# Performance work log

Hardware: AMD Instinct MI355X
Metric: run time of the kernel (lower is better)

Reference implementation:

```python
import jax, jax.numpy as jnp
import numpy as np

N, IN_DIM, OUT_DIM, BATCH = 8192, 128, 128, 4


def _glorot(key, shape):
    lim = float(np.sqrt(6.0 / (shape[0] + shape[1])))
    return jax.random.uniform(key, shape, jnp.float32, -lim, lim)


def setup_inputs() -> dict:
    key = jax.random.key(0)
    ks = jax.random.split(key, 16)
    inp = {
        "x": jax.random.normal(ks[0], (BATCH, N, IN_DIM), jnp.float32),
        "L0": jax.random.normal(ks[1], (N, N), jnp.float32) / np.sqrt(N),
        "L1": jax.random.normal(ks[2], (N, N), jnp.float32) / np.sqrt(N),
        "L2": jax.random.normal(ks[3], (N, N), jnp.float32) / np.sqrt(N),
        "L3": jax.random.normal(ks[4], (N, N), jnp.float32) / np.sqrt(N),
    }
    # 8 GCN layers: (branch b, layer l) -> W_bl, bias_bl
    kidx = 5
    for b in range(4):
        for l in range(2):
            d_in = IN_DIM if l == 0 else OUT_DIM
            inp[f"W{b}{l}"] = _glorot(ks[kidx], (d_in, OUT_DIM))
            inp[f"b{b}{l}"] = jnp.zeros((OUT_DIM,), jnp.float32)
            kidx += 1
    return inp


def _gcn_block(L, x, W, b):
    # support = L @ x  (graph propagation), then dense transform + ReLU
    support = jnp.einsum("nm,bmf->bnf", L, x)  # [B, N, F_in]
    return jax.nn.relu(support @ W + b)        # [B, N, F_out]


def reference(x, L0, L1, L2, L3,
              W00, b00, W01, b01,
              W10, b10, W11, b11,
              W20, b20, W21, b21,
              W30, b30, W31, b31):
    x0 = _gcn_block(L0, _gcn_block(L0, x, W00, b00), W01, b01)
    x1 = _gcn_block(L1, _gcn_block(L1, x, W10, b10), W11, b11)
    x2 = _gcn_block(L2, _gcn_block(L2, x, W20, b20), W21, b21)
    x3 = _gcn_block(L3, _gcn_block(L3, x, W30, b30), W31, b31)
    return (x0, x1, x2, x3)
```

## Files before the change

kernel.cpp:

```cpp
#include <hip/hip_runtime.h>
#include <stdint.h>


typedef short bf16x8 __attribute__((ext_vector_type(8)));
typedef float f32x4 __attribute__((ext_vector_type(4)));

static __device__ __forceinline__ unsigned short f2bf(float f) {
  __bf16 h = (__bf16)f;
  return __builtin_bit_cast(unsigned short, h);
}
static __device__ __forceinline__ unsigned int pack2(float a, float b) {
  return (unsigned int)f2bf(a) | ((unsigned int)f2bf(b) << 16);
}
static __device__ __forceinline__ bf16x8 cvt8(float4 lo, float4 hi) {
  bf16x8 r;
  r[0] = (short)f2bf(lo.x); r[1] = (short)f2bf(lo.y);
  r[2] = (short)f2bf(lo.z); r[3] = (short)f2bf(lo.w);
  r[4] = (short)f2bf(hi.x); r[5] = (short)f2bf(hi.y);
  r[6] = (short)f2bf(hi.z); r[7] = (short)f2bf(hi.w);
  return r;
}

#define GLOAD16(g, l)                                                                  \
  __builtin_amdgcn_global_load_lds((const __attribute__((address_space(1))) void*)(g), \
                                   (__attribute__((address_space(3))) void*)(l), 16, 0, 0)

struct WPtrs { const float* w[8]; };
__global__ __launch_bounds__(256)
void prep_w(WPtrs p, unsigned short* __restrict__ wt) {
  const int s = blockIdx.x;
  const float* W = p.w[s];
  unsigned short* dst = wt + s * 16384;
  for (int i = threadIdx.x; i < 16384; i += 256) {
    const int fi = i >> 7, fo = i & 127;
    dst[fo * 128 + fi] = f2bf(W[i]);
  }
}

template <int AFP32>
__global__ __launch_bounds__(256)
void small_gemm(const float* __restrict__ x, const unsigned short* __restrict__ H1m,
                const unsigned short* __restrict__ WT, unsigned short* __restrict__ Z) {
  __shared__ unsigned short Sa[128 * 136];

  const int t = threadIdx.x, lane = t & 63, wave = t >> 6;
  const int l15 = lane & 15, lk = (lane >> 4) * 8;
  const int wm = (wave >> 1) * 64, wn = (wave & 1) * 64;
  const int mt = blockIdx.x, br = blockIdx.y;
  const int batch = mt >> 6, node0 = (mt & 63) * 128;

  {
    const int row = t >> 1, seg = (t & 1) * 64;
    if (AFP32) {
      const float4* src = (const float4*)(x + ((size_t)batch * 8192 + node0 + row) * 128 + seg);
      uint4* dst = (uint4*)&Sa[row * 136 + seg];
#pragma unroll
      for (int i = 0; i < 8; ++i) {
        float4 a = src[i * 2], b = src[i * 2 + 1];
        uint4 v;
        v.x = pack2(a.x, a.y); v.y = pack2(a.z, a.w);
        v.z = pack2(b.x, b.y); v.w = pack2(b.z, b.w);
        dst[i] = v;
      }
    } else {
      const uint4* src = (const uint4*)(H1m + ((size_t)(br * 4 + batch) * 8192 + node0 + row) * 128 + seg);
      uint4* dst = (uint4*)&Sa[row * 136 + seg];
#pragma unroll
      for (int i = 0; i < 8; ++i) dst[i] = src[i];
    }
  }
  __syncthreads();

  const unsigned short* WTb = WT + (size_t)(2 * br + (AFP32 ? 0 : 1)) * 16384;
  f32x4 acc[4][4];
#pragma unroll
  for (int i = 0; i < 4; ++i)
#pragma unroll
    for (int j = 0; j < 4; ++j) acc[i][j] = f32x4{0.f, 0.f, 0.f, 0.f};

#pragma unroll
  for (int kk = 0; kk < 4; ++kk) {
    bf16x8 av[4], wv[4];
#pragma unroll
    for (int mi = 0; mi < 4; ++mi)
      av[mi] = *(const bf16x8*)&Sa[(wm + mi * 16 + l15) * 136 + kk * 32 + lk];
#pragma unroll
    for (int ni = 0; ni < 4; ++ni)
      wv[ni] = *(const bf16x8*)&WTb[(wn + ni * 16 + l15) * 128 + kk * 32 + lk];
#pragma unroll
    for (int mi = 0; mi < 4; ++mi)
#pragma unroll
      for (int ni = 0; ni < 4; ++ni)
        acc[mi][ni] = __builtin_amdgcn_mfma_f32_16x16x32_bf16(av[mi], wv[ni], acc[mi][ni], 0, 0, 0);
  }

#pragma unroll
  for (int mi = 0; mi < 4; ++mi) {
#pragma unroll
    for (int ni = 0; ni < 4; ++ni) {
      const int row0 = wm + mi * 16 + (lane >> 4) * 4;
      const int col  = wn + ni * 16 + l15;
      uint2 pv;
      pv.x = pack2(acc[mi][ni][0], acc[mi][ni][1]);
      pv.y = pack2(acc[mi][ni][2], acc[mi][ni][3]);
      *(uint2*)(Z + ((size_t)br * 512 + batch * 128 + col) * 8192 + node0 + row0) = pv;
    }
  }
}

struct BigArgs {
  const float* L[4];
  const float* bias[4];
  const unsigned short* Z;
  void* Dst;
};

template <int LAYER>
__global__ __launch_bounds__(512, 2)
void big_gemm(BigArgs a) {
  extern __shared__ char smem[];

  const int t = threadIdx.x, lane = t & 63, wave = t >> 6;
  const int l15 = lane & 15;
  const int wm = (wave >> 2) * 128, wn = (wave & 3) * 64;

  const int bid = blockIdx.x;
  const int work = (bid & 7) * 32 + (bid >> 3);
  const int nb = work & 1, mt = (work >> 1) & 31, br = work >> 6;
  const int mbase = mt * 256;

  const float* A = a.L[br];
  const float* bias = a.bias[br];
  const unsigned short* Zb = a.Z + (size_t)br * (512 * 8192);

  const int c0 = 2 * (lane & 1);
  const int akey = (lane >> 2) & 3;
  const float* aBase = A + (size_t)(mbase + wave * 32 + (lane >> 1)) * 8192 + c0 * 8;
  char* aLane = smem + (wave * 32 + (lane >> 1)) * 64;
  const unsigned short* bG = Zb + (size_t)(nb * 256 + wave * 32 + (lane >> 2)) * 8192
                                + ((lane & 3) ^ ((lane >> 3) & 3)) * 8;
  char* bWave = smem + 65536 + wave * 2048;

  const int aoff = (((lane >> 4) ^ ((lane >> 1) & 3)) & 7) * 16;

  f32x4 acc[8][4];
#pragma unroll
  for (int i = 0; i < 8; ++i)
#pragma unroll
    for (int j = 0; j < 4; ++j) acc[i][j] = f32x4{0.f, 0.f, 0.f, 0.f};

  float4 ra[4], rb[4];

#define GLB(s)                                              \
  do {                                                      \
    const unsigned short* bp = bG + (size_t)(s) * 32;       \
    char* bl = bWave + ((s) & 3) * 16384;                   \
    GLOAD16(bp, bl);                                        \
    GLOAD16(bp + 16 * 8192, bl + 1024);                     \
  } while (0)

#define LOADA(s, R)                                         \
  do {                                                      \
    const float* ap = aBase + (size_t)(s) * 32;             \
    R[0] = *(const float4*)(ap);                            \
    R[1] = *(const float4*)(ap + 4);                        \
    R[2] = *(const float4*)(ap + 8);                        \
    R[3] = *(const float4*)(ap + 12);                       \
  } while (0)

#define WRITEA(s, R)                                                        \
  do {                                                                      \
    char* al = aLane + ((s) & 3) * 16384;                                   \
    *(bf16x8*)(al + ((c0 ^ akey) * 16)) = cvt8(R[0], R[1]);                 \
    *(bf16x8*)(al + (((c0 + 1) ^ akey) * 16)) = cvt8(R[2], R[3]);           \
  } while (0)

#define MFMA_HALF(NLO)                                                                         \
  do {                                                                                         \
    __builtin_amdgcn_s_setprio(1);                                                             \
    _Pragma("unroll") for (int mi = 0; mi < 8; ++mi) {                                         \
      acc[mi][NLO] = __builtin_amdgcn_mfma_f32_16x16x32_bf16(av[mi], bv[0], acc[mi][NLO], 0, 0, 0); \
      acc[mi][NLO + 1] = __builtin_amdgcn_mfma_f32_16x16x32_bf16(av[mi], bv[1], acc[mi][NLO + 1], 0, 0, 0); \
    }                                                                                          \
    __builtin_amdgcn_s_setprio(0);                                                             \
  } while (0)

#define ITER(T_, PREV_, NEXT_, VMSTR_, DO_GLB_, DO_LOADA_, DO_WRITEA_)                  \
  do {                                                                                  \
    asm volatile("s_waitcnt lgkmcnt(0)" ::: "memory");                                  \
    __builtin_amdgcn_s_barrier();                                                       \
    asm volatile("" ::: "memory");                                                      \
    if (DO_GLB_) GLB((T_) + 3);                                                         \
    if (DO_LOADA_) LOADA((T_) + 2, NEXT_);                                              \
    const char* ab = smem + ((T_) & 3) * 16384;                                         \
    const char* bb = smem + 65536 + ((T_) & 3) * 16384;                                 \
    bf16x8 av[8], bv[2];                                                                \
    _Pragma("unroll") for (int mi = 0; mi < 8; ++mi)                                    \
        av[mi] = *(const bf16x8*)(ab + (wm + mi * 16 + l15) * 64 + aoff);               \
    bv[0] = *(const bf16x8*)(bb + (wn + l15) * 64 + aoff);                              \
    bv[1] = *(const bf16x8*)(bb + (wn + 16 + l15) * 64 + aoff);                         \
    MFMA_HALF(0);                                                                       \
    if (DO_WRITEA_) {                                                                   \
      asm volatile("s_waitcnt " VMSTR_ ::: "memory");                                   \
      WRITEA((T_) + 1, PREV_);                                                          \
    }                                                                                   \
    bv[0] = *(const bf16x8*)(bb + (wn + 32 + l15) * 64 + aoff);                         \
    bv[1] = *(const bf16x8*)(bb + (wn + 48 + l15) * 64 + aoff);                         \
    MFMA_HALF(2);                                                                       \
  } while (0)

  GLB(0); GLB(1); GLB(2);
  LOADA(0, ra); LOADA(1, rb);
  WRITEA(0, ra);

  for (int tt = 0; tt < 252; tt += 2) {
    ITER(tt,     rb, ra, "vmcnt(6)", 1, 1, 1);
    ITER(tt + 1, ra, rb, "vmcnt(6)", 1, 1, 1);
  }
  ITER(252, rb, ra, "vmcnt(6)", 1, 1, 1);
  ITER(253, ra, rb, "vmcnt(4)", 0, 1, 1);
  ITER(254, rb, ra, "vmcnt(0)", 0, 0, 1);
  {
    asm volatile("s_waitcnt lgkmcnt(0)" ::: "memory");
    __builtin_amdgcn_s_barrier();
    asm volatile("" ::: "memory");
    const char* ab = smem + (255 & 3) * 16384;
    const char* bb = smem + 65536 + (255 & 3) * 16384;
    bf16x8 av[8], bv[2];
#pragma unroll
    for (int mi = 0; mi < 8; ++mi)
      av[mi] = *(const bf16x8*)(ab + (wm + mi * 16 + l15) * 64 + aoff);
    bv[0] = *(const bf16x8*)(bb + (wn + l15) * 64 + aoff);
    bv[1] = *(const bf16x8*)(bb + (wn + 16 + l15) * 64 + aoff);
    MFMA_HALF(0);
    bv[0] = *(const bf16x8*)(bb + (wn + 32 + l15) * 64 + aoff);
    bv[1] = *(const bf16x8*)(bb + (wn + 48 + l15) * 64 + aoff);
    MFMA_HALF(2);
  }
#undef ITER
#undef MFMA_HALF
#undef WRITEA
#undef LOADA
#undef GLB

  asm volatile("s_waitcnt lgkmcnt(0)" ::: "memory");
  __builtin_amdgcn_s_barrier();
  asm volatile("" ::: "memory");

  unsigned short* S16 = (unsigned short*)smem;
  float* S32 = (float*)smem;

#pragma unroll
  for (int h = 0; h < 2; ++h) {
    if (((wave >> 1) & 1) == h) {
#pragma unroll
      for (int mi = 0; mi < 8; ++mi) {
#pragma unroll
        for (int ni = 0; ni < 4; ++ni) {
          const int row0 = wm + mi * 16 + (lane >> 4) * 4;
          const int col  = (wave & 1) * 64 + ni * 16 + l15;
          const float bvv = bias[col];
#pragma unroll
          for (int r = 0; r < 4; ++r) {
            const float v = fmaxf(acc[mi][ni][r] + bvv, 0.f);
            if (LAYER == 0) S16[(row0 + r) * 136 + col] = f2bf(v);
            else            S32[(row0 + r) * 128 + col] = v;
          }
        }
      }
    }
    __syncthreads();
    const int batch = nb * 2 + h;
    const int row = t >> 1, seg = (t & 1) * 64;
    if (LAYER == 0) {
      unsigned short* Dst = (unsigned short*)a.Dst;
      const uint4* src = (const uint4*)&S16[row * 136 + seg];
      uint4* dst = (uint4*)(Dst + ((size_t)(br * 4 + batch) * 8192 + mbase + row) * 128 + seg);
#pragma unroll
      for (int i = 0; i < 8; ++i) dst[i] = src[i];
    } else {
      float* Dst = (float*)a.Dst;
      const float4* src = (const float4*)&S32[row * 128 + seg];
      float4* dst = (float4*)(Dst + ((size_t)(br * 4 + batch) * 8192 + mbase + row) * 128 + seg);
#pragma unroll
      for (int i = 0; i < 16; ++i) dst[i] = src[i];
    }
    __syncthreads();
  }
}

extern "C" void kernel_launch(void* const* d_in, const int* in_sizes, int n_in,
                              void* d_out, int out_size, void* d_ws, size_t ws_size,
                              hipStream_t stream) {
  const float* x = (const float*)d_in[0];
  unsigned short* Z   = (unsigned short*)d_ws;
  unsigned short* H1m = Z + (size_t)4 * 512 * 8192;
  unsigned short* WT  = H1m + (size_t)4 * 4 * 8192 * 128;
  float* out = (float*)d_out;

  static int attr_done = 0;
  if (!attr_done) {
    hipFuncSetAttribute((const void*)big_gemm<0>, hipFuncAttributeMaxDynamicSharedMemorySize, 131072);
    hipFuncSetAttribute((const void*)big_gemm<1>, hipFuncAttributeMaxDynamicSharedMemorySize, 131072);
    attr_done = 1;
  }

  WPtrs wp;
  for (int b = 0; b < 4; ++b) {
    wp.w[b * 2 + 0] = (const float*)d_in[5 + b * 4 + 0];
    wp.w[b * 2 + 1] = (const float*)d_in[5 + b * 4 + 2];
  }
  prep_w<<<8, 256, 0, stream>>>(wp, WT);

  BigArgs a0, a1;
  for (int b = 0; b < 4; ++b) {
    a0.L[b] = (const float*)d_in[1 + b];
    a1.L[b] = (const float*)d_in[1 + b];
    a0.bias[b] = (const float*)d_in[6 + b * 4];
    a1.bias[b] = (const float*)d_in[8 + b * 4];
  }
  a0.Z = Z; a0.Dst = (void*)H1m;
  a1.Z = Z; a1.Dst = (void*)out;

  small_gemm<1><<<dim3(256, 4), 256, 0, stream>>>(x, nullptr, WT, Z);
  big_gemm<0><<<256, 512, 131072, stream>>>(a0);
  small_gemm<0><<<dim3(256, 4), 256, 0, stream>>>(nullptr, H1m, WT, Z);
  big_gemm<1><<<256, 512, 131072, stream>>>(a1);
}
```

Measured before the change: 1.032 ms.

## Rewrite big GEMM main loop with 32x32x16 MFMA and 64-wide K stages

Replaces the 16x16x32 MFMA tiling with 32x32x16 bf16 MFMAs, so each wave holds eight 32x32 accumulators. The K loop now stages 64-wide A and B slices, with A double-buffered in registers and B triple-buffered in LDS, using 160KB of shared memory and new XOR swizzles. The point is to cut LDS fragment reads per FLOP and issue denser MFMA work. In exchange it adds two barriers per phase, drops the min-2-blocks launch bound, and needs more LDS per block.

Result: slower. 1.776 ms (+72.1%).

```diff
diff --git a/kernel.cpp b/kernel.cpp
--- a/kernel.cpp
+++ b/kernel.cpp
@@ -3,7 +3,8 @@
 
 
 typedef short bf16x8 __attribute__((ext_vector_type(8)));
-typedef float f32x4 __attribute__((ext_vector_type(4)));
+typedef float f32x4  __attribute__((ext_vector_type(4)));
+typedef float f32x16 __attribute__((ext_vector_type(16)));
 
 static __device__ __forceinline__ unsigned short f2bf(float f) {
   __bf16 h = (__bf16)f;
@@ -116,12 +117,12 @@
 };
 
 template <int LAYER>
-__global__ __launch_bounds__(512, 2)
+__global__ __launch_bounds__(512)
 void big_gemm(BigArgs a) {
   extern __shared__ char smem[];
 
   const int t = threadIdx.x, lane = t & 63, wave = t >> 6;
-  const int l15 = lane & 15;
+  const int l31 = lane & 31, hk = lane >> 5;
   const int wm = (wave >> 2) * 128, wn = (wave & 3) * 64;
 
   const int bid = blockIdx.x;
@@ -133,141 +134,137 @@
   const float* bias = a.bias[br];
   const unsigned short* Zb = a.Z + (size_t)br * (512 * 8192);
 
-  const int c0 = 2 * (lane & 1);
-  const int akey = (lane >> 2) & 3;
-  const float* aBase = A + (size_t)(mbase + wave * 32 + (lane >> 1)) * 8192 + c0 * 8;
-  char* aLane = smem + (wave * 32 + (lane >> 1)) * 64;
-  const unsigned short* bG = Zb + (size_t)(nb * 256 + wave * 32 + (lane >> 2)) * 8192
-                                + ((lane & 3) ^ ((lane >> 3) & 3)) * 8;
-  char* bWave = smem + 65536 + wave * 2048;
-
-  const int aoff = (((lane >> 4) ^ ((lane >> 1) & 3)) & 7) * 16;
-
-  f32x4 acc[8][4];
-#pragma unroll
-  for (int i = 0; i < 8; ++i)
-#pragma unroll
-    for (int j = 0; j < 4; ++j) acc[i][j] = f32x4{0.f, 0.f, 0.f, 0.f};
-
-  float4 ra[4], rb[4];
-
-#define GLB(s)                                              \
-  do {                                                      \
-    const unsigned short* bp = bG + (size_t)(s) * 32;       \
-    char* bl = bWave + ((s) & 3) * 16384;                   \
-    GLOAD16(bp, bl);                                        \
-    GLOAD16(bp + 16 * 8192, bl + 1024);                     \
+  const int arow = t >> 1, ah = t & 1;
+  const float* aG = A + (size_t)(mbase + arow) * 8192 + ah * 32;
+  const int awBase = arow * 128, awKey = arow & 7, ah4 = ah * 4;
+  const int brow = lane >> 3;
+  const unsigned short* bG = Zb + (size_t)(nb * 256 + wave * 32 + brow) * 8192
+                                + ((lane & 7) ^ (brow & 7)) * 8;
+  const int bW = wave * 4096;
+
+  const int aBase = (wm + l31) * 128;
+  const int bBase = (wn + l31) * 128;
+  const int key7 = l31 & 7;
+
+  f32x16 c00{}, c01{}, c10{}, c11{}, c20{}, c21{}, c30{}, c31{};
+  float4 E[8], O[8];
+  bf16x8 av0, av1, av2, av3, bv0, bv1;
+
+#define A_LD(SET, KOFF, q) do {                              \
+    const float* _p = aG + (KOFF) + (q) * 8;                 \
+    SET[2 * (q)]     = *(const float4*)_p;                   \
+    SET[2 * (q) + 1] = *(const float4*)(_p + 4); } while (0)
+
+#define A_WR(SET, SLOT, q) do {                              \
+    *(bf16x8*)(smem + (SLOT) * 32768 + awBase +              \
+               (((ah4 + (q)) ^ awKey) * 16)) =               \
+        cvt8(SET[2 * (q)], SET[2 * (q) + 1]); } while (0)
+
+#define B_ST(KOFF, BOFFD, q) do {                            \
+    const unsigned short* _p = bG + (KOFF) + (size_t)(q) * 8 * 8192;  \
+    GLOAD16(_p, smem + 65536 + (BOFFD) + bW + (q) * 1024); } while (0)
+
+#define RD_FRAGS(ASLOT, BOFF, q) do {                        \
+    const int _ch = (((2 * (q)) + hk) ^ key7) * 16;          \
+    const char* _ap = smem + (ASLOT) + aBase + _ch;          \
+    av0 = *(const bf16x8*)(_ap);                             \
+    av1 = *(const bf16x8*)(_ap + 4096);                      \
+    av2 = *(const bf16x8*)(_ap + 8192);                      \
+    av3 = *(const bf16x8*)(_ap + 12288);                     \
+    const char* _bp = smem + 65536 + (BOFF) + bBase + _ch;   \
+    bv0 = *(const bf16x8*)(_bp);                             \
+    bv1 = *(const bf16x8*)(_bp + 4096); } while (0)
+
+#define DO_MFMA() do {                                                     \
+    __builtin_amdgcn_s_setprio(1);                                         \
+    c00 = __builtin_amdgcn_mfma_f32_32x32x16_bf16(av0, bv0, c00, 0, 0, 0); \
+    c01 = __builtin_amdgcn_mfma_f32_32x32x16_bf16(av0, bv1, c01, 0, 0, 0); \
+    c10 = __builtin_amdgcn_mfma_f32_32x32x16_bf16(av1, bv0, c10, 0, 0, 0); \
+    c11 = __builtin_amdgcn_mfma_f32_32x32x16_bf16(av1, bv1, c11, 0, 0, 0); \
+    c20 = __builtin_amdgcn_mfma_f32_32x32x16_bf16(av2, bv0, c20, 0, 0, 0); \
+    c21 = __builtin_amdgcn_mfma_f32_32x32x16_bf16(av2, bv1, c21, 0, 0, 0); \
+    c30 = __builtin_amdgcn_mfma_f32_32x32x16_bf16(av3, bv0, c30, 0, 0, 0); \
+    c31 = __builtin_amdgcn_mfma_f32_32x32x16_bf16(av3, bv1, c31, 0, 0, 0); \
+    __builtin_amdgcn_s_setprio(0); } while (0)
+
+#define VM12 asm volatile("s_waitcnt vmcnt(12)" ::: "memory")
+#define VM0  asm volatile("s_waitcnt vmcnt(0)" ::: "memory")
+#define NOSTG (void)0
+
+#define PHASE(ASLOT, BOFF, q, STAGES, VM) do {               \
+    STAGES;                                                  \
+    RD_FRAGS(ASLOT, BOFF, q);                                \
+    VM;                                                      \
+    asm volatile("s_waitcnt lgkmcnt(0)" ::: "memory");       \
+    __builtin_amdgcn_s_barrier();                            \
+    DO_MFMA();                                               \
+    __builtin_amdgcn_s_barrier();                            \
   } while (0)
 
-#define LOADA(s, R)                                         \
-  do {                                                      \
-    const float* ap = aBase + (size_t)(s) * 32;             \
-    R[0] = *(const float4*)(ap);                            \
-    R[1] = *(const float4*)(ap + 4);                        \
-    R[2] = *(const float4*)(ap + 8);                        \
-    R[3] = *(const float4*)(ap + 12);                       \
-  } while (0)
-
-#define WRITEA(s, R)                                                        \
-  do {                                                                      \
-    char* al = aLane + ((s) & 3) * 16384;                                   \
-    *(bf16x8*)(al + ((c0 ^ akey) * 16)) = cvt8(R[0], R[1]);                 \
-    *(bf16x8*)(al + (((c0 + 1) ^ akey) * 16)) = cvt8(R[2], R[3]);           \
-  } while (0)
-
-#define MFMA_HALF(NLO)                                                                         \
-  do {                                                                                         \
-    __builtin_amdgcn_s_setprio(1);                                                             \
-    _Pragma("unroll") for (int mi = 0; mi < 8; ++mi) {                                         \
-      acc[mi][NLO] = __builtin_amdgcn_mfma_f32_16x16x32_bf16(av[mi], bv[0], acc[mi][NLO], 0, 0, 0); \
-      acc[mi][NLO + 1] = __builtin_amdgcn_mfma_f32_16x16x32_bf16(av[mi], bv[1], acc[mi][NLO + 1], 0, 0, 0); \
-    }                                                                                          \
-    __builtin_amdgcn_s_setprio(0);                                                             \
-  } while (0)
-
-#define ITER(T_, PREV_, NEXT_, VMSTR_, DO_GLB_, DO_LOADA_, DO_WRITEA_)                  \
-  do {                                                                                  \
-    asm volatile("s_waitcnt lgkmcnt(0)" ::: "memory");                                  \
-    __builtin_amdgcn_s_barrier();                                                       \
-    asm volatile("" ::: "memory");                                                      \
-    if (DO_GLB_) GLB((T_) + 3);                                                         \
-    if (DO_LOADA_) LOADA((T_) + 2, NEXT_);                                              \
-    const char* ab = smem + ((T_) & 3) * 16384;                                         \
-    const char* bb = smem + 65536 + ((T_) & 3) * 16384;                                 \
-    bf16x8 av[8], bv[2];                                                                \
-    _Pragma("unroll") for (int mi = 0; mi < 8; ++mi)                                    \
-        av[mi] = *(const bf16x8*)(ab + (wm + mi * 16 + l15) * 64 + aoff);               \
-    bv[0] = *(const bf16x8*)(bb + (wn + l15) * 64 + aoff);                              \
-    bv[1] = *(const bf16x8*)(bb + (wn + 16 + l15) * 64 + aoff);                         \
-    MFMA_HALF(0);                                                                       \
-    if (DO_WRITEA_) {                                                                   \
-      asm volatile("s_waitcnt " VMSTR_ ::: "memory");                                   \
-      WRITEA((T_) + 1, PREV_);                                                          \
-    }                                                                                   \
-    bv[0] = *(const bf16x8*)(bb + (wn + 32 + l15) * 64 + aoff);                         \
-    bv[1] = *(const bf16x8*)(bb + (wn + 48 + l15) * 64 + aoff);                         \
-    MFMA_HALF(2);                                                                       \
-  } while (0)
-
-  GLB(0); GLB(1); GLB(2);
-  LOADA(0, ra); LOADA(1, rb);
-  WRITEA(0, ra);
-
-  for (int tt = 0; tt < 252; tt += 2) {
-    ITER(tt,     rb, ra, "vmcnt(6)", 1, 1, 1);
-    ITER(tt + 1, ra, rb, "vmcnt(6)", 1, 1, 1);
-  }
-  ITER(252, rb, ra, "vmcnt(6)", 1, 1, 1);
-  ITER(253, ra, rb, "vmcnt(4)", 0, 1, 1);
-  ITER(254, rb, ra, "vmcnt(0)", 0, 0, 1);
-  {
-    asm volatile("s_waitcnt lgkmcnt(0)" ::: "memory");
-    __builtin_amdgcn_s_barrier();
-    asm volatile("" ::: "memory");
-    const char* ab = smem + (255 & 3) * 16384;
-    const char* bb = smem + 65536 + (255 & 3) * 16384;
-    bf16x8 av[8], bv[2];
-#pragma unroll
-    for (int mi = 0; mi < 8; ++mi)
-      av[mi] = *(const bf16x8*)(ab + (wm + mi * 16 + l15) * 64 + aoff);
-    bv[0] = *(const bf16x8*)(bb + (wn + l15) * 64 + aoff);
-    bv[1] = *(const bf16x8*)(bb + (wn + 16 + l15) * 64 + aoff);
-    MFMA_HALF(0);
-    bv[0] = *(const bf16x8*)(bb + (wn + 32 + l15) * 64 + aoff);
-    bv[1] = *(const bf16x8*)(bb + (wn + 48 + l15) * 64 + aoff);
-    MFMA_HALF(2);
-  }
-#undef ITER
-#undef MFMA_HALF
-#undef WRITEA
-#undef LOADA
-#undef GLB
-
+  int o0 = 0, o1 = 32768, o2 = 65536;
+  A_LD(E, 0, 0); A_LD(E, 0, 1); A_LD(E, 0, 2); A_LD(E, 0, 3);
+  A_LD(O, 64, 0); A_LD(O, 64, 1); A_LD(O, 64, 2); A_LD(O, 64, 3);
+  B_ST(0, 0, 0); B_ST(0, 0, 1); B_ST(0, 0, 2); B_ST(0, 0, 3);
+  B_ST(64, 32768, 0); B_ST(64, 32768, 1); B_ST(64, 32768, 2); B_ST(64, 32768, 3);
+  asm volatile("s_waitcnt vmcnt(16)" ::: "memory");
+  A_WR(E, 0, 0); A_WR(E, 0, 1); A_WR(E, 0, 2); A_WR(E, 0, 3);
+  asm volatile("s_waitcnt vmcnt(4)" ::: "memory");
   asm volatile("s_waitcnt lgkmcnt(0)" ::: "memory");
   __builtin_amdgcn_s_barrier();
-  asm volatile("" ::: "memory");
+
+  int kE = 128, kO = 192;
+
+  for (int b = 0; b < 63; ++b) {
+    PHASE(0, o0, 0, { A_LD(E, kE, 0); A_WR(O, 1, 0); B_ST(kE, o2, 0); }, NOSTG);
+    PHASE(0, o0, 1, { A_LD(E, kE, 1); A_WR(O, 1, 1); B_ST(kE, o2, 1); }, NOSTG);
+    PHASE(0, o0, 2, { A_LD(E, kE, 2); A_WR(O, 1, 2); B_ST(kE, o2, 2); }, NOSTG);
+    PHASE(0, o0, 3, { A_LD(E, kE, 3); A_WR(O, 1, 3); B_ST(kE, o2, 3); }, VM12);
+    PHASE(32768, o1, 0, { A_LD(O, kO, 0); A_WR(E, 0, 0); B_ST(kO, o0, 0); }, NOSTG);
+    PHASE(32768, o1, 1, { A_LD(O, kO, 1); A_WR(E, 0, 1); B_ST(kO, o0, 1); }, NOSTG);
+    PHASE(32768, o1, 2, { A_LD(O, kO, 2); A_WR(E, 0, 2); B_ST(kO, o0, 2); }, NOSTG);
+    PHASE(32768, o1, 3, { A_LD(O, kO, 3); A_WR(E, 0, 3); B_ST(kO, o0, 3); }, VM12);
+    const int n0 = o2, n1 = o0, n2 = o1;
+    o0 = n0; o1 = n1; o2 = n2;
+    kE += 128; kO += 128;
+  }
+
+  PHASE(0, o0, 0, { A_WR(O, 1, 0); }, NOSTG);
+  PHASE(0, o0, 1, { A_WR(O, 1, 1); }, NOSTG);
+  PHASE(0, o0, 2, { A_WR(O, 1, 2); }, NOSTG);
+  PHASE(0, o0, 3, { A_WR(O, 1, 3); }, VM0);
+  PHASE(32768, o1, 0, NOSTG, NOSTG);
+  PHASE(32768, o1, 1, NOSTG, NOSTG);
+  PHASE(32768, o1, 2, NOSTG, NOSTG);
+  PHASE(32768, o1, 3, NOSTG, NOSTG);
+
+#undef PHASE
+#undef DO_MFMA
+#undef RD_FRAGS
+#undef B_ST
+#undef A_WR
+#undef A_LD
 
   unsigned short* S16 = (unsigned short*)smem;
   float* S32 = (float*)smem;
 
+#define EPI(AM, BN, ACC) do {                                               \
+    const int col = (wave & 1) * 64 + (BN) * 32 + l31;                      \
+    const float bvv = bias[col];                                            \
+    _Pragma("unroll") for (int r = 0; r < 16; ++r) {                        \
+      const int row = wm + (AM) * 32 + (r & 3) + 8 * (r >> 2) + 4 * hk;     \
+      float v = ACC[r] + bvv;                                               \
+      v = fmaxf(v, 0.f);                                                    \
+      if (LAYER == 0) S16[row * 136 + col] = f2bf(v);                       \
+      else            S32[row * 128 + col] = v;                             \
+    } } while (0)
+
 #pragma unroll
   for (int h = 0; h < 2; ++h) {
     if (((wave >> 1) & 1) == h) {
-#pragma unroll
-      for (int mi = 0; mi < 8; ++mi) {
-#pragma unroll
-        for (int ni = 0; ni < 4; ++ni) {
-          const int row0 = wm + mi * 16 + (lane >> 4) * 4;
-          const int col  = (wave & 1) * 64 + ni * 16 + l15;
-          const float bvv = bias[col];
-#pragma unroll
-          for (int r = 0; r < 4; ++r) {
-            const float v = fmaxf(acc[mi][ni][r] + bvv, 0.f);
-            if (LAYER == 0) S16[(row0 + r) * 136 + col] = f2bf(v);
-            else            S32[(row0 + r) * 128 + col] = v;
-          }
-        }
-      }
+      EPI(0, 0, c00); EPI(0, 1, c01);
+      EPI(1, 0, c10); EPI(1, 1, c11);
+      EPI(2, 0, c20); EPI(2, 1, c21);
+      EPI(3, 0, c30); EPI(3, 1, c31);
     }
     __syncthreads();
     const int batch = nb * 2 + h;
@@ -287,6 +284,7 @@
     }
     __syncthreads();
   }
+#undef EPI
 }
 
 extern "C" void kernel_launch(void* const* d_in, const int* in_sizes, int n_in,
@@ -300,8 +298,8 @@
 
   static int attr_done = 0;
   if (!attr_done) {
-    hipFuncSetAttribute((const void*)big_gemm<0>, hipFuncAttributeMaxDynamicSharedMemorySize, 131072);
-    hipFuncSetAttribute((const void*)big_gemm<1>, hipFuncAttributeMaxDynamicSharedMemorySize, 131072);
+    hipFuncSetAttribute((const void*)big_gemm<0>, hipFuncAttributeMaxDynamicSharedMemorySize, 163840);
+    hipFuncSetAttribute((const void*)big_gemm<1>, hipFuncAttributeMaxDynamicSharedMemorySize, 163840);
     attr_done = 1;
   }
 
@@ -323,7 +321,7 @@
   a1.Z = Z; a1.Dst = (void*)out;
 
   small_gemm<1><<<dim3(256, 4), 256, 0, stream>>>(x, nullptr, WT, Z);
-  big_gemm<0><<<256, 512, 131072, stream>>>(a0);
+  big_gemm<0><<<256, 512, 163840, stream>>>(a0);
   small_gemm<0><<<dim3(256, 4), 256, 0, stream>>>(nullptr, H1m, WT, Z);
-  big_gemm<1><<<256, 512, 131072, stream>>>(a1);
-}
+  big_gemm<1><<<256, 512, 163840, stream>>>(a1);
+}
```
